# Kernel optimization log

Hardware: AMD Instinct MI355X
Metric: run time of the kernel (lower is better)

The kernel has to match this reference:

```python
import jax, jax.numpy as jnp
import numpy as np
import math

B, N, IN_DIM = 128, 100, 8
E, H, FF, L = 512, 8, 2048, 6
DH = E // H
MAX_STEPS = int(N * 1.5)
EPS = 1e-5

def _ln(x, g, b):
    mu = x.mean(-1, keepdims=True)
    var = ((x - mu) ** 2).mean(-1, keepdims=True)
    return (x - mu) / jnp.sqrt(var + EPS) * g + b

def _mha(q_in, k_in, v_in, wq, bq, wk, bk, wv, bv, wo, bo):
    Bq, Sq = q_in.shape[0], q_in.shape[1]
    q = (q_in @ wq + bq).reshape(Bq, Sq, H, DH)
    k = (k_in @ wk + bk).reshape(Bq, -1, H, DH)
    v = (v_in @ wv + bv).reshape(Bq, -1, H, DH)
    s = jnp.einsum('bqhd,bkhd->bhqk', q, k) / math.sqrt(DH)
    a = jax.nn.softmax(s, axis=-1)
    o = jnp.einsum('bhqk,bkhd->bqhd', a, v).reshape(Bq, Sq, E)
    return o @ wo + bo

def setup_inputs():
    key = jax.random.key(0)
    keys = iter(jax.random.split(key, 64))
    def nrm(shape, s=0.02):
        return jax.random.normal(next(keys), shape, jnp.float32) * s
    d = {}
    d['node_features'] = jax.random.normal(next(keys), (B, N, IN_DIM), jnp.float32)
    d['edge_weights'] = jax.random.uniform(next(keys), (B, N, N), jnp.float32)
    pos = np.arange(N)[:, None].astype(np.float32)
    div = np.exp(np.arange(0, E, 2).astype(np.float32) * (-math.log(10000.0) / E))
    pe = np.zeros((N, E), np.float32)
    pe[:, 0::2] = np.sin(pos * div); pe[:, 1::2] = np.cos(pos * div)
    d['pe'] = jnp.asarray(pe)
    d['in_w'] = nrm((IN_DIM, E)); d['in_b'] = jnp.zeros((E,), jnp.float32)
    for nm in ['enc_wq', 'enc_wk', 'enc_wv', 'enc_wo']:
        d[nm] = nrm((L, E, E))
    for nm in ['enc_bq', 'enc_bk', 'enc_bv', 'enc_bo']:
        d[nm] = jnp.zeros((L, E), jnp.float32)
    d['enc_w1'] = nrm((L, E, FF)); d['enc_b1'] = jnp.zeros((L, FF), jnp.float32)
    d['enc_w2'] = nrm((L, FF, E)); d['enc_b2'] = jnp.zeros((L, E), jnp.float32)
    d['enc_ln1g'] = jnp.ones((L, E), jnp.float32); d['enc_ln1b'] = jnp.zeros((L, E), jnp.float32)
    d['enc_ln2g'] = jnp.ones((L, E), jnp.float32); d['enc_ln2b'] = jnp.zeros((L, E), jnp.float32)
    d['lstm_wih'] = nrm((E, 4 * E)); d['lstm_whh'] = nrm((E, 4 * E))
    d['lstm_bih'] = jnp.zeros((4 * E,), jnp.float32); d['lstm_bhh'] = jnp.zeros((4 * E,), jnp.float32)
    for nm in ['dec_wq', 'dec_wk', 'dec_wv', 'dec_wo', 'dec_pw']:
        d[nm] = nrm((E, E))
    for nm in ['dec_bq', 'dec_bk', 'dec_bv', 'dec_bo', 'dec_pb']:
        d[nm] = jnp.zeros((E,), jnp.float32)
    d['dec_lng'] = jnp.ones((E,), jnp.float32); d['dec_lnb'] = jnp.zeros((E,), jnp.float32)
    d['shortcut_bonus'] = jnp.asarray(5.0, jnp.float32)
    d['revisit_penalty'] = jnp.asarray(-0.5, jnp.float32)
    d['done_w'] = nrm((E, 1)); d['done_b'] = jnp.zeros((1,), jnp.float32)
    return d

def _forward(node_features, edge_weights, pe, in_w, in_b, enc_wq, enc_bq, enc_wk, enc_bk, enc_wv, enc_bv, enc_wo, enc_bo, enc_w1, enc_b1, enc_w2, enc_b2, enc_ln1g, enc_ln1b, enc_ln2g, enc_ln2b, lstm_wih, lstm_whh, lstm_bih, lstm_bhh, dec_wq, dec_bq, dec_wk, dec_bk, dec_wv, dec_bv, dec_wo, dec_bo, dec_pw, dec_pb, dec_lng, dec_lnb, shortcut_bonus, revisit_penalty, done_w, done_b):
    # ---- Encoder (dropout = eval-mode identity) ----
    x = node_features @ in_w + in_b + pe[:N]
    for l in range(L):
        attn = _mha(x, x, x, enc_wq[l], enc_bq[l], enc_wk[l], enc_bk[l], enc_wv[l], enc_bv[l], enc_wo[l], enc_bo[l])
        x = _ln(x + attn, enc_ln1g[l], enc_ln1b[l])
        ff = jax.nn.relu(x @ enc_w1[l] + enc_b1[l]) @ enc_w2[l] + enc_b2[l]
        x = _ln(x + ff, enc_ln2g[l], enc_ln2b[l])
    node_emb = x  # [B, N, E]

    ar = jnp.arange(N)
    ew_to_first = edge_weights[:, :, 0]  # dist(mid -> node 0), [B, N]

    def step_fn(carry, step):
        h, c, ctx, visited, ucount, complete, all_vis, first, prev = carry
        # LSTMCell, torch gate order (i, f, g, o)
        gates = ctx @ lstm_wih + lstm_bih + h @ lstm_whh + lstm_bhh
        i_g, f_g, g_g, o_g = jnp.split(gates, 4, axis=-1)
        c2 = jax.nn.sigmoid(f_g) * c + jax.nn.sigmoid(i_g) * jnp.tanh(g_g)
        h2 = jax.nn.sigmoid(o_g) * jnp.tanh(c2)
        # greedy done-predictor: stop if sigmoid(logit) > 0.5 once tour can be closed
        done_p = jax.nn.sigmoid(h2 @ done_w + done_b)[:, 0]
        eligible = (~complete) & (ucount >= N) & (step >= N)
        complete = complete | (eligible & (done_p > 0.5))
        # DecoderStep: 1-query attention over node embeddings
        a = _mha(h2[:, None, :], node_emb, node_emb, dec_wq, dec_bq, dec_wk, dec_bk, dec_wv, dec_bv, dec_wo, dec_bo)[:, 0]
        a = _ln(a, dec_lng, dec_lnb)
        logits = a @ dec_pw + dec_pb
        scores = jnp.einsum('be,bne->bn', logits, node_emb)
        # revisit penalty while tour incomplete (vectorized masked_fill_)
        scores = jnp.where((~all_vis)[:, None] & visited, revisit_penalty, scores)
        # shortcut bonus once all nodes visited (vectorized gather over edge_weights)
        ew_prev = jnp.take_along_axis(edge_weights, prev[:, None, None], axis=1)[:, 0, :]  # [B, N] row dist(prev -> *)
        direct = ew_prev[:, :1]                      # dist(prev -> 0)
        via = ew_prev + ew_to_first                  # dist(prev -> mid) + dist(mid -> 0)
        bonus = jnp.where(via < direct, shortcut_bonus * (direct - via) / direct, 0.0)
        scores = scores + jnp.where(all_vis[:, None], bonus, 0.0)
        # completed tours: force return to first node
        scores = jnp.where(complete[:, None], -1e9, scores)
        scores = jnp.where(complete[:, None] & (ar[None, :] == first[:, None]), 100.0, scores)
        probs = jax.nn.softmax(scores, axis=1)
        curr = jnp.argmax(probs, axis=1).astype(jnp.int32)  # greedy selection
        logp = jnp.log(jnp.take_along_axis(probs, curr[:, None], 1)[:, 0] + 1e-10)
        first = jnp.where(step == 0, curr, first)
        # state updates (guarded by active, as in the torch per-batch loop)
        active = ~complete
        cur_mask = ar[None, :] == curr[:, None]
        newly = active & ~jnp.take_along_axis(visited, curr[:, None], 1)[:, 0]
        ucount = ucount + newly.astype(jnp.int32)
        visited = visited | (active[:, None] & cur_mask)
        all_vis = all_vis | (ucount >= N)
        ctx2 = jnp.take_along_axis(node_emb, curr[:, None, None], axis=1)[:, 0, :]
        return (h2, c2, ctx2, visited, ucount, complete, all_vis, first, curr), (curr, logp)

    carry0 = (jnp.zeros((B, E), jnp.float32), jnp.zeros((B, E), jnp.float32), node_emb.mean(1),
              jnp.zeros((B, N), bool), jnp.zeros((B,), jnp.int32),
              jnp.zeros((B,), bool), jnp.zeros((B,), bool),
              jnp.zeros((B,), jnp.int32), jnp.zeros((B,), jnp.int32))
    carry, (tours, logps) = jax.lax.scan(step_fn, carry0, jnp.arange(MAX_STEPS))
    complete, first = carry[5], carry[7]
    # final forced step (step == max_steps in torch): incomplete tours return to first node, logp = 0
    final_node = jnp.where(complete, jnp.int32(0), first)
    tours = jnp.concatenate([tours, final_node[None]], 0)                 # [MAX_STEPS+1, B]
    logps = jnp.concatenate([logps, jnp.zeros((1, B), jnp.float32)], 0)   # [MAX_STEPS+1, B]
    return logps, tours

def reference(node_features, edge_weights, pe, in_w, in_b, enc_wq, enc_bq, enc_wk, enc_bk, enc_wv, enc_bv, enc_wo, enc_bo, enc_w1, enc_b1, enc_w2, enc_b2, enc_ln1g, enc_ln1b, enc_ln2g, enc_ln2b, lstm_wih, lstm_whh, lstm_bih, lstm_bhh, dec_wq, dec_bq, dec_wk, dec_bk, dec_wv, dec_bv, dec_wo, dec_bo, dec_pw, dec_pb, dec_lng, dec_lnb, shortcut_bonus, revisit_penalty, done_w, done_b):
    return _forward(node_features, edge_weights, pe, in_w, in_b, enc_wq, enc_bq, enc_wk, enc_bk, enc_wv, enc_bv, enc_wo, enc_bo, enc_w1, enc_b1, enc_w2, enc_b2, enc_ln1g, enc_ln1b, enc_ln2g, enc_ln2b, lstm_wih, lstm_whh, lstm_bih, lstm_bhh, dec_wq, dec_bq, dec_wk, dec_bk, dec_wv, dec_bv, dec_wo, dec_bo, dec_pw, dec_pb, dec_lng, dec_lnb, shortcut_bonus, revisit_penalty, done_w, done_b)
```

## Files before the change

kernel.cpp:

```cpp
#include <hip/hip_runtime.h>
#include <math.h>

#define Bb 128
#define Nn 100
#define Ee 512
#define Hh 8
#define DHd 64
#define FFf 2048
#define Ll 6
#define STEPS 150

typedef _Float16 h8 __attribute__((ext_vector_type(8)));
typedef _Float16 h4 __attribute__((ext_vector_type(4)));
typedef float f4 __attribute__((ext_vector_type(4)));

template<bool RELU, bool BIAS, bool OUTF32, bool SPLITK>
__global__ __launch_bounds__(256) void mgemm_k(
    const _Float16* __restrict__ Ah, const _Float16* __restrict__ Al, int lda,
    const _Float16* __restrict__ Bh, const _Float16* __restrict__ Bl, int ldb,
    float* __restrict__ C, _Float16* __restrict__ Ch, _Float16* __restrict__ Cl,
    int ldc, const float* __restrict__ bias, int K, int kc, int Mtot)
{
  __shared__ _Float16 sm[4 * 5120];
  _Float16* sAh = sm;
// ... 47 lines not shown
      }
    __syncthreads();
  }

  float* Cz = OUTF32 ? (C + (SPLITK ? (size_t)blockIdx.z * (size_t)Mtot * ldc : (size_t)0)) : C;
  int rb = m0 + wm * 64 + kg * 4;
  int cb = n0 + wn * 64 + m16;
#pragma unroll
  for (int j = 0; j < 4; ++j) {
    int col = cb + j * 16;
    float bv = BIAS ? bias[col] : 0.f;
#pragma unroll
    for (int i = 0; i < 4; ++i) {
#pragma unroll
      for (int r = 0; r < 4; ++r) {
        float v = acc[i][j][r] + bv;
        if (RELU) v = fmaxf(v, 0.f);
        int row = rb + i * 16 + r;
        if (OUTF32) {
          Cz[(size_t)row * ldc + col] = v;
        } else {
          _Float16 hh = (_Float16)v;
          Ch[(size_t)row * ldc + col] = hh;
          Cl[(size_t)row * ldc + col] = (_Float16)(v - (float)hh);
        }
      }
    }
  }
}

__global__ __launch_bounds__(256) void wconv_k(
    const float* __restrict__ W, int K, int N,
    _Float16* __restrict__ Th, _Float16* __restrict__ Tl)
{
  __shared__ float t[32][33];
  int n0 = blockIdx.x * 32, k0 = blockIdx.y * 32;
  int tid = threadIdx.x;
  int r = tid >> 3, c4 = (tid & 7) * 4;
  float4 v = *(const float4*)(W + (size_t)(k0 + r) * N + n0 + c4);
  t[r][c4 + 0] = v.x; t[r][c4 + 1] = v.y; t[r][c4 + 2] = v.z; t[r][c4 + 3] = v.w;
  __syncthreads();
  h4 hi, lo;
#pragma unroll
  for (int i = 0; i < 4; ++i) {
    float x = t[c4 + i][r];
    _Float16 hh = (_Float16)x;
    hi[i] = hh;
    lo[i] = (_Float16)(x - (float)hh);
  }
  *(h4*)(Th + (size_t)(n0 + r) * K + k0 + c4) = hi;
  *(h4*)(Tl + (size_t)(n0 + r) * K + k0 + c4) = lo;
}

__global__ __launch_bounds__(256) void reduce4_k(
    const float* __restrict__ P, const float* __restrict__ bias, float* __restrict__ out)
{
  int idx = blockIdx.x * 256 + threadIdx.x;
  const size_t S = 3200ull * 512;
  float v = P[idx] + P[idx + S] + P[idx + 2 * S] + P[idx + 3 * S] + bias[idx & 511];
  out[idx] = v;
}

__global__ __launch_bounds__(256) void input_proj_k(
    const float* __restrict__ nf, const float* __restrict__ inw,
    const float* __restrict__ inb, const float* __restrict__ pe,
    float* __restrict__ x, _Float16* __restrict__ xh, _Float16* __restrict__ xl)
{
  int idx = blockIdx.x * 256 + threadIdx.x;
  int bn = idx >> 9, e = idx & 511;
  int n = bn - (bn / Nn) * Nn;
  const float* fr = nf + (size_t)bn * 8;
  float s = inb[e] + pe[(size_t)n * 512 + e];
#pragma unroll
  for (int i = 0; i < 8; ++i) s += fr[i] * inw[(size_t)i * 512 + e];
  x[idx] = s;
  _Float16 hh = (_Float16)s;
  xh[idx] = hh;
  xl[idx] = (_Float16)(s - (float)hh);
}

__global__ __launch_bounds__(256) void ln_k(
    const float* __restrict__ xin, const float* __restrict__ yin,
    const float* __restrict__ g, const float* __restrict__ bb,
    float* __restrict__ out, _Float16* __restrict__ oh, _Float16* __restrict__ ol)
{
  int row = blockIdx.x, t = threadIdx.x;
  __shared__ float red[256];
  size_t base = (size_t)row * 512;
  float v0 = xin[base + t] + yin[base + t];
  float v1 = xin[base + 256 + t] + yin[base + 256 + t];
  red[t] = v0 + v1;
  __syncthreads();
  for (int o = 128; o > 0; o >>= 1) { if (t < o) red[t] += red[t + o]; __syncthreads(); }
  float mu = red[0] * (1.f / 512.f);
  __syncthreads();
  float d0 = v0 - mu, d1 = v1 - mu;
  red[t] = d0 * d0 + d1 * d1;
  __syncthreads();
  for (int o = 128; o > 0; o >>= 1) { if (t < o) red[t] += red[t + o]; __syncthreads(); }
  float inv = 1.f / sqrtf(red[0] * (1.f / 512.f) + 1e-5f);
  float y0 = d0 * inv * g[t] + bb[t];
  float y1 = d1 * inv * g[t + 256] + bb[t + 256];
  out[base + t] = y0;
  out[base + 256 + t] = y1;
  _Float16 h0 = (_Float16)y0, h1 = (_Float16)y1;
  oh[base + t] = h0;           ol[base + t] = (_Float16)(y0 - (float)h0);
// ... 43 lines not shown
#pragma unroll
    for (int c = 0; c < 7; ++c) {
      int i = i0 + r, j = j0 + c;
      if (i < Nn && j < Nn) p[i * 104 + j] = s[r][c] * 0.125f;
    }
  __syncthreads();
  int w = t >> 6, lane = t & 63;
  for (int i = w; i < Nn; i += 4) {
    float x0 = p[i * 104 + lane];
    float x1 = (lane < 36) ? p[i * 104 + 64 + lane] : -3.4e38f;
    float mx = fmaxf(x0, x1);
    for (int msk = 32; msk; msk >>= 1) mx = fmaxf(mx, __shfl_xor(mx, msk));
    float e0 = expf(x0 - mx);
    float e1 = (lane < 36) ? expf(x1 - mx) : 0.f;
    float ss = e0 + e1;
    for (int msk = 32; msk; msk >>= 1) ss += __shfl_xor(ss, msk);
    p[i * 104 + lane] = e0 / ss;
    if (lane < 36) p[i * 104 + 64 + lane] = e1 / ss;
  }
  __syncthreads();
  int d0 = tj * 4;
  float oa[7][4];
#pragma unroll
  for (int r = 0; r < 7; ++r)
#pragma unroll
    for (int c = 0; c < 4; ++c) oa[r][c] = 0.f;
  for (int j = 0; j < Nn; ++j) {
    float pr[7];
#pragma unroll
    for (int r = 0; r < 7; ++r) pr[r] = p[(i0 + r) * 104 + j];
    float4 vv = *(const float4*)(vg + (size_t)j * 512 + d0);
#pragma unroll
    for (int r = 0; r < 7; ++r) {
      oa[r][0] += pr[r] * vv.x; oa[r][1] += pr[r] * vv.y;
      oa[r][2] += pr[r] * vv.z; oa[r][3] += pr[r] * vv.w;
    }
  }
  size_t ob = ((size_t)b * Nn) * 512 + h * 64 + d0;
#pragma unroll
  for (int r = 0; r < 7; ++r)
    if (i0 + r < Nn) {
      h4 hv, lv;
#pragma unroll
      for (int c = 0; c < 4; ++c) {
        _Float16 hh = (_Float16)oa[r][c];
        hv[c] = hh;
        lv[c] = (_Float16)(oa[r][c] - (float)hh);
      }
      *(h4*)(oh + ob + (size_t)(i0 + r) * 512) = hv;
      *(h4*)(ol + ob + (size_t)(i0 + r) * 512) = lv;
    }
}

template<int BM, int BN, int BK, int TM, int TN>
__global__ __launch_bounds__(256) void gemm_k(
    const float* __restrict__ A, int lda,
    const float* __restrict__ B1, const float* __restrict__ B2, int splitB, int ldb,
    float* __restrict__ C, int ldc, int M, int N, int K, int kChunk)
{
  __shared__ __align__(16) float As[BK][BM + 4];
  __shared__ __align__(16) float Bs[BK][BN + 4];
  const int tid = threadIdx.x;
  const int m0 = blockIdx.y * BM;
  const int n0 = blockIdx.x * BN;
  const int k0 = blockIdx.z * kChunk;
  const int kEnd = k0 + kChunk;
  constexpr int TCOLS = BN / TN;
  const int tm = tid / TCOLS;
  const int tn = tid % TCOLS;
  float acc[TM][TN];
#pragma unroll
  for (int i = 0; i < TM; ++i)
#pragma unroll
    for (int j = 0; j < TN; ++j) acc[i][j] = 0.f;

  for (int kt = k0; kt < kEnd; kt += BK) {
    constexpr int A4 = BM * BK / 4;
    for (int c = tid; c < A4; c += 256) {
      int mm = c / (BK / 4);
      int k4 = (c % (BK / 4)) * 4;
      float4 av = *(const float4*)(A + (size_t)(m0 + mm) * lda + kt + k4);
      As[k4 + 0][mm] = av.x;
      As[k4 + 1][mm] = av.y;
      As[k4 + 2][mm] = av.z;
      As[k4 + 3][mm] = av.w;
    }
    constexpr int B4 = BK * BN / 4;
    for (int c = tid; c < B4; c += 256) {
      int kk = c / (BN / 4);
      int n4 = (c % (BN / 4)) * 4;
      int kgi = kt + kk;
      const float* Brow = (kgi < splitB) ? (B1 + (size_t)kgi * ldb)
                                         : (B2 + (size_t)(kgi - splitB) * ldb);
      *(float4*)&Bs[kk][n4] = *(const float4*)(Brow + n0 + n4);
    }
    __syncthreads();
#pragma unroll
    for (int kk = 0; kk < BK; ++kk) {
      float a[TM], b[TN];
#pragma unroll
      for (int i = 0; i < TM; ++i) a[i] = As[kk][tm * TM + i];
#pragma unroll
      for (int j = 0; j < TN; ++j) b[j] = Bs[kk][tn * TN + j];
#pragma unroll
      for (int i = 0; i < TM; ++i)
#pragma unroll
        for (int j = 0; j < TN; ++j)
          acc[i][j] += a[i] * b[j];
    }
    __syncthreads();
  }

  float* Cout = C + (size_t)blockIdx.z * (size_t)M * ldc;
#pragma unroll
  for (int i = 0; i < TM; ++i) {
    int m = m0 + tm * TM + i;
#pragma unroll
    for (int j = 0; j < TN; j += 4) {
      int n = n0 + tn * TN + j;
      float4 r;
      r.x = acc[i][j + 0]; r.y = acc[i][j + 1]; r.z = acc[i][j + 2]; r.w = acc[i][j + 3];
      *(float4*)(Cout + (size_t)m * ldc + n) = r;
    }
  }
}

__global__ __launch_bounds__(256) void init_k(
    const float* __restrict__ emb, float* __restrict__ ctxh, float* __restrict__ cbuf,
    int* visited, int* ucount, int* complete, int* allvis, int* first, int* prev,
    float* out)
{
  int b = blockIdx.x, t = threadIdx.x;
#pragma unroll
  for (int r = 0; r < 2; ++r) {
    int e = t + 256 * r;
    float s = 0.f;
    for (int i = 0; i < Nn; ++i) s += emb[((size_t)b * Nn + i) * 512 + e];
    ctxh[(size_t)b * 1024 + e] = s / 100.f;
    ctxh[(size_t)b * 1024 + 512 + e] = 0.f;
    cbuf[(size_t)b * 512 + e] = 0.f;
  }
  if (t < Nn) visited[b * Nn + t] = 0;
  if (t == 0) {
    ucount[b] = 0; complete[b] = 0; allvis[b] = 0; first[b] = 0; prev[b] = 0;
    out[150 * Bb + b] = 0.f;
  }
}

__device__ __forceinline__ float sigm(float x) { return 1.f / (1.f + expf(-x)); }

__global__ __launch_bounds__(256) void lstm_pw_k(
    const float* __restrict__ gP, const float* __restrict__ bih, const float* __restrict__ bhh,
    float* __restrict__ ctxh, float* __restrict__ cbuf,
    const float* __restrict__ done_w, const float* __restrict__ done_b,
    int* complete, const int* ucount, int step)
{
  int b = blockIdx.x, t = threadIdx.x;
  __shared__ float red[256];
  const float* g0 = gP + (size_t)b * 2048;
  const float* g1 = gP + 262144 + (size_t)b * 2048;
  float dsum = 0.f;
#pragma unroll
  for (int r = 0; r < 2; ++r) {
    int e = t + 256 * r;
    float ig = g0[e] + g1[e] + bih[e] + bhh[e];
    float fg = g0[e + 512] + g1[e + 512] + bih[e + 512] + bhh[e + 512];
    float gg = g0[e + 1024] + g1[e + 1024] + bih[e + 1024] + bhh[e + 1024];
    float og = g0[e + 1536] + g1[e + 1536] + bih[e + 1536] + bhh[e + 1536];
    float cprev = cbuf[(size_t)b * 512 + e];
    float c2 = sigm(fg) * cprev + sigm(ig) * tanhf(gg);
    float h2 = sigm(og) * tanhf(c2);
    cbuf[(size_t)b * 512 + e] = c2;
    ctxh[(size_t)b * 1024 + 512 + e] = h2;
    dsum += h2 * done_w[e];
  }
  red[t] = dsum; __syncthreads();
  for (int o = 128; o > 0; o >>= 1) { if (t < o) red[t] += red[t + o]; __syncthreads(); }
  if (t == 0) {
    float z = red[0] + done_b[0];
    if (!complete[b] && ucount[b] >= Nn && step >= Nn && z > 0.f) complete[b] = 1;
  }
}

__global__ __launch_bounds__(128) void dec_attn_k(
    const float* __restrict__ qP, const float* __restrict__ bq,
    const float* __restrict__ Kd, const float* __restrict__ Vd,
    float* __restrict__ o)
{
  int bh = blockIdx.x; int b = bh >> 3, h = bh & 7;
  int t = threadIdx.x;
  __shared__ float qh[64];
  __shared__ float p[100];
  __shared__ float red[128];
  if (t < 64) {
    float s = bq[h * 64 + t];
#pragma unroll
    for (int s8 = 0; s8 < 8; ++s8) s += qP[(size_t)s8 * 65536 + (size_t)b * 512 + h * 64 + t];
    qh[t] = s;
  }
  __syncthreads();
  float scv = -3.4e38f;
  if (t < Nn) {
    const float* kr = Kd + ((size_t)b * Nn + t) * 512 + h * 64;
    float s = 0.f;
#pragma unroll
    for (int d = 0; d < 64; ++d) s += qh[d] * kr[d];
    scv = s * 0.125f;
  }
  red[t] = scv; __syncthreads();
  for (int o2 = 64; o2 > 0; o2 >>= 1) { if (t < o2) red[t] = fmaxf(red[t], red[t + o2]); __syncthreads(); }
  float m = red[0]; __syncthreads();
  float ex = (t < Nn) ? expf(scv - m) : 0.f;
  red[t] = ex; __syncthreads();
  for (int o2 = 64; o2 > 0; o2 >>= 1) { if (t < o2) red[t] += red[t + o2]; __syncthreads(); }
  float Z = red[0];
  if (t < Nn) p[t] = ex / Z;
  __syncthreads();
  if (t < 64) {
    float acc = 0.f;
    const float* vr = Vd + (size_t)b * Nn * 512 + h * 64 + t;
    for (int j = 0; j < Nn; ++j) acc += p[j] * vr[(size_t)j * 512];
    o[(size_t)b * 512 + h * 64 + t] = acc;
  }
}

__global__ __launch_bounds__(256) void dec_ln_k(
    const float* __restrict__ woP, const float* __restrict__ bo,
    const float* __restrict__ g, const float* __restrict__ bb,
    float* __restrict__ out)
{
  int b = blockIdx.x, t = threadIdx.x;
  __shared__ float red[256];
  float v[2];
#pragma unroll
  for (int r = 0; r < 2; ++r) {
    int e = t + 256 * r;
    float s = bo[e];
#pragma unroll
    for (int s8 = 0; s8 < 8; ++s8) s += woP[(size_t)s8 * 65536 + (size_t)b * 512 + e];
    v[r] = s;
  }
  red[t] = v[0] + v[1]; __syncthreads();
  for (int o = 128; o > 0; o >>= 1) { if (t < o) red[t] += red[t + o]; __syncthreads(); }
  float mu = red[0] * (1.f / 512.f);
  __syncthreads();
  float d0 = v[0] - mu, d1 = v[1] - mu;
  red[t] = d0 * d0 + d1 * d1; __syncthreads();
  for (int o = 128; o > 0; o >>= 1) { if (t < o) red[t] += red[t + o]; __syncthreads(); }
  float inv = 1.f / sqrtf(red[0] * (1.f / 512.f) + 1e-5f);
  out[(size_t)b * 512 + t] = d0 * inv * g[t] + bb[t];
  out[(size_t)b * 512 + t + 256] = d1 * inv * g[t + 256] + bb[t + 256];
}

__global__ __launch_bounds__(256) void select_k(
    const float* __restrict__ pwP, const float* __restrict__ pb,
    const float* __restrict__ emb, const float* __restrict__ ew,
    int* visited, int* ucount, int* complete, int* allvis, int* first, int* prev,
    float* __restrict__ ctxh, float* __restrict__ out,
    const float* __restrict__ sb_p, const float* __restrict__ rp_p, int step)
{
  int b = blockIdx.x, t = threadIdx.x;
  __shared__ float logits[512];
  __shared__ float sc[128];
  __shared__ float red[256];
  __shared__ int redi[256];
#pragma unroll
  for (int r = 0; r < 2; ++r) {
    int e = t + 256 * r;
    float s = pb[e];
#pragma unroll
    for (int s8 = 0; s8 < 8; ++s8) s += pwP[(size_t)s8 * 65536 + (size_t)b * 512 + e];
    logits[e] = s;
  }
  __syncthreads();
  if (t < Nn) {
    const float* er = emb + ((size_t)b * Nn + t) * 512;
    float s = 0.f;
    for (int e = 0; e < 512; ++e) s += logits[e] * er[e];
    int av = allvis[b];
    if (!av && visited[b * Nn + t]) s = rp_p[0];
    if (av) {
      int pv = prev[b];
      float direct = ew[(size_t)b * 10000 + (size_t)pv * 100];
      float via = ew[(size_t)b * 10000 + (size_t)pv * 100 + t] + ew[(size_t)b * 10000 + (size_t)t * 100];
      if (via < direct) s += sb_p[0] * (direct - via) / direct;
    }
    if (complete[b]) s = (t == first[b]) ? 100.f : -1e9f;
    sc[t] = s;
  }
  __syncthreads();
  float vv = (t < Nn) ? sc[t] : -3.4e38f;
  int ii = (t < Nn) ? t : 0x7fffffff;
  red[t] = vv; redi[t] = ii;
  __syncthreads();
  for (int o = 128; o > 0; o >>= 1) {
    if (t < o) {
      float v2 = red[t + o]; int i2 = redi[t + o];
      if (v2 > red[t] || (v2 == red[t] && i2 < redi[t])) { red[t] = v2; redi[t] = i2; }
    }
    __syncthreads();
  }
  float m = red[0];
  int curr = redi[0];
  __syncthreads();
  float ex = (t < Nn) ? expf(sc[t] - m) : 0.f;
  red[t] = ex; __syncthreads();
  for (int o = 128; o > 0; o >>= 1) { if (t < o) red[t] += red[t + o]; __syncthreads(); }
  float Z = red[0];
  if (t == 0) {
    float pcur = expf(sc[curr] - m) / Z;
    out[step * Bb + b] = logf(pcur + 1e-10f);
    out[(151 + step) * Bb + b] = (float)curr;
    if (!complete[b]) {
      if (!visited[b * Nn + curr]) ucount[b] = ucount[b] + 1;
      visited[b * Nn + curr] = 1;
    }
    if (ucount[b] >= Nn) allvis[b] = 1;
    if (step == 0) first[b] = curr;
    prev[b] = curr;
  }
  const float* src = emb + ((size_t)b * Nn + curr) * 512;
  ctxh[(size_t)b * 1024 + t] = src[t];
  ctxh[(size_t)b * 1024 + t + 256] = src[t + 256];
}

__global__ void final_k(const int* complete, const int* first, float* out)
{
  int b = threadIdx.x;
  out[(151 + 150) * Bb + b] = complete[b] ? 0.f : (float)first[b];
}

extern "C" void kernel_launch(void* const* d_in, const int* in_sizes, int n_in,
                              void* d_out, int out_size, void* d_ws, size_t ws_size,
                              hipStream_t stream)
{
  const float* nf      = (const float*)d_in[0];
  const float* ew      = (const float*)d_in[1];
  const float* pe      = (const float*)d_in[2];
  const float* in_w    = (const float*)d_in[3];
  const float* in_b    = (const float*)d_in[4];
  const float* enc_wq  = (const float*)d_in[5];
  const float* enc_wk  = (const float*)d_in[6];
  const float* enc_wv  = (const float*)d_in[7];
  const float* enc_wo  = (const float*)d_in[8];
  const float* enc_bq  = (const float*)d_in[9];
  const float* enc_bk  = (const float*)d_in[10];
  const float* enc_bv  = (const float*)d_in[11];
  const float* enc_bo  = (const float*)d_in[12];
  const float* enc_w1  = (const float*)d_in[13];
  const float* enc_b1  = (const float*)d_in[14];
  const float* enc_w2  = (const float*)d_in[15];
  const float* enc_b2  = (const float*)d_in[16];
  const float* ln1g    = (const float*)d_in[17];
  const float* ln1b    = (const float*)d_in[18];
  const float* ln2g    = (const float*)d_in[19];
  const float* ln2b    = (const float*)d_in[20];
  const float* wih     = (const float*)d_in[21];
  const float* whh     = (const float*)d_in[22];
  const float* bih     = (const float*)d_in[23];
  const float* bhh     = (const float*)d_in[24];
  const float* dwq     = (const float*)d_in[25];
  const float* dwk     = (const float*)d_in[26];
  const float* dwv     = (const float*)d_in[27];
  const float* dwo     = (const float*)d_in[28];
  const float* dpw     = (const float*)d_in[29];
  const float* dbq     = (const float*)d_in[30];
  const float* dbk     = (const float*)d_in[31];
  const float* dbv     = (const float*)d_in[32];
  const float* dbo     = (const float*)d_in[33];
  const float* dpb     = (const float*)d_in[34];
  const float* dlng    = (const float*)d_in[35];
  const float* dlnb    = (const float*)d_in[36];
  const float* sbp     = (const float*)d_in[37];
  const float* rpp     = (const float*)d_in[38];
  const float* done_w  = (const float*)d_in[39];
  const float* done_b  = (const float*)d_in[40];
  float* out = (float*)d_out;

  const size_t SZ = 12800ull * 512;
  float* ws = (float*)d_ws;
  float* x   = ws;
  float* xq  = x + SZ;
  float* xk  = xq + SZ;
  float* xv  = xk + SZ;
  _Float16* xh = (_Float16*)(xv + SZ);
  _Float16* xl = xh + SZ;
  _Float16* oh = xl + SZ;
  _Float16* ol = oh + SZ;
  _Float16* wb = ol + SZ;
  _Float16* wqh = wb;               _Float16* wql = wqh + 262144;
  _Float16* wkh = wql + 262144;     _Float16* wkl = wkh + 262144;
  _Float16* wvh = wkl + 262144;     _Float16* wvl = wvh + 262144;
  _Float16* woh_ = wvl + 262144;    _Float16* wol_ = woh_ + 262144;
  _Float16* w1h = wol_ + 262144;    _Float16* w1l = w1h + 1048576;
  _Float16* w2h = w1l + 1048576;    _Float16* w2l = w2h + 1048576;
  float* ctxh   = (float*)(w2l + 1048576);
  float* cbuf   = ctxh + 131072;
  float* gatesP = cbuf + 65536;
  float* qP     = gatesP + 524288;
  float* woP    = qP + 524288;
  float* pwP    = woP + 524288;
  float* abuf   = pwP + 524288;
  float* dbuf   = abuf + 65536;
  int* ivis     = (int*)(dbuf + 65536);
  int* ucount   = ivis + 12800;
  int* complete = ucount + 128;
  int* allvis   = complete + 128;
  int* first    = allvis + 128;
  int* prev     = first + 128;

  input_proj_k<<<25600, 256, 0, stream>>>(nf, in_w, in_b, pe, x, xh, xl);

  for (int l = 0; l < Ll; ++l) {
    const float* wq = enc_wq + (size_t)l * 262144;
    const float* wk = enc_wk + (size_t)l * 262144;
    const float* wv = enc_wv + (size_t)l * 262144;
    const float* wo = enc_wo + (size_t)l * 262144;
    const float* bq = enc_bq + (size_t)l * 512;
    const float* bk = enc_bk + (size_t)l * 512;
    const float* bv = enc_bv + (size_t)l * 512;
    const float* bo = enc_bo + (size_t)l * 512;
    const float* w1 = enc_w1 + (size_t)l * 1048576;
    const float* b1 = enc_b1 + (size_t)l * 2048;
    const float* w2 = enc_w2 + (size_t)l * 1048576;
    const float* b2 = enc_b2 + (size_t)l * 512;

    wconv_k<<<dim3(16, 16), 256, 0, stream>>>(wq, 512, 512, wqh, wql);
    wconv_k<<<dim3(16, 16), 256, 0, stream>>>(wk, 512, 512, wkh, wkl);
    wconv_k<<<dim3(16, 16), 256, 0, stream>>>(wv, 512, 512, wvh, wvl);
    wconv_k<<<dim3(16, 16), 256, 0, stream>>>(wo, 512, 512, woh_, wol_);
    wconv_k<<<dim3(64, 16), 256, 0, stream>>>(w1, 512, 2048, w1h, w1l);
    wconv_k<<<dim3(16, 64), 256, 0, stream>>>(w2, 2048, 512, w2h, w2l);

    mgemm_k<false, true, true, false><<<dim3(4, 100), 256, 0, stream>>>(
        xh, xl, 512, wqh, wql, 512, xq, nullptr, nullptr, 512, bq, 512, 0, 0);
    mgemm_k<false, true, true, false><<<dim3(4, 100), 256, 0, stream>>>(
        xh, xl, 512, wkh, wkl, 512, xk, nullptr, nullptr, 512, bk, 512, 0, 0);
    mgemm_k<false, true, true, false><<<dim3(4, 100), 256, 0, stream>>>(
        xh, xl, 512, wvh, wvl, 512, xv, nullptr, nullptr, 512, bv, 512, 0, 0);
    enc_attn_k<<<1024, 256, 0, stream>>>(xq, xk, xv, oh, ol);
    mgemm_k<false, true, true, false><<<dim3(4, 100), 256, 0, stream>>>(
        oh, ol, 512, woh_, wol_, 512, xq, nullptr, nullptr, 512, bo, 512, 0, 0);
    ln_k<<<12800, 256, 0, stream>>>(x, xq, ln1g + l * 512, ln1b + l * 512, x, xh, xl);
    for (int c = 0; c < 4; ++c) {
      mgemm_k<true, true, false, false><<<dim3(16, 25), 256, 0, stream>>>(
          xh + (size_t)c * 3200 * 512, xl + (size_t)c * 3200 * 512, 512,
          w1h, w1l, 512, nullptr, oh, ol, 2048, b1, 512, 0, 0);
      mgemm_k<false, false, true, true><<<dim3(4, 25, 4), 256, 0, stream>>>(
          oh, ol, 2048, w2h, w2l, 2048, xv, nullptr, nullptr, 512,
          nullptr, 2048, 512, 3200);
      reduce4_k<<<6400, 256, 0, stream>>>(xv, b2, xq + (size_t)c * 3200 * 512);
    }
    ln_k<<<12800, 256, 0, stream>>>(x, xq, ln2g + l * 512, ln2b + l * 512, x, xh, xl);
  }

  wconv_k<<<dim3(16, 16), 256, 0, stream>>>(dwk, 512, 512, wqh, wql);
  wconv_k<<<dim3(16, 16), 256, 0, stream>>>(dwv, 512, 512, wkh, wkl);
  mgemm_k<false, true, true, false><<<dim3(4, 100), 256, 0, stream>>>(
      xh, xl, 512, wqh, wql, 512, xk, nullptr, nullptr, 512, dbk, 512, 0, 0);
  mgemm_k<false, true, true, false><<<dim3(4, 100), 256, 0, stream>>>(
      xh, xl, 512, wkh, wkl, 512, xv, nullptr, nullptr, 512, dbv, 512, 0, 0);
  init_k<<<128, 256, 0, stream>>>(x, ctxh, cbuf, ivis, ucount, complete, allvis, first, prev, out);

  for (int step = 0; step < STEPS; ++step) {
    gemm_k<32, 64, 16, 2, 4><<<dim3(32, 4, 2), 256, 0, stream>>>(
        ctxh, 1024, wih, whh, 512, 2048, gatesP, 2048, 128, 2048, 1024, 512);
    lstm_pw_k<<<128, 256, 0, stream>>>(gatesP, bih, bhh, ctxh, cbuf, done_w, done_b,
                                       complete, ucount, step);
    gemm_k<32, 64, 16, 2, 4><<<dim3(8, 4, 8), 256, 0, stream>>>(
        ctxh + 512, 1024, dwq, dwq, 1 << 30, 512, qP, 512, 128, 512, 512, 64);
    dec_attn_k<<<1024, 128, 0, stream>>>(qP, dbq, xk, xv, dbuf);
    gemm_k<32, 64, 16, 2, 4><<<dim3(8, 4, 8), 256, 0, stream>>>(
        dbuf, 512, dwo, dwo, 1 << 30, 512, woP, 512, 128, 512, 512, 64);
    dec_ln_k<<<128, 256, 0, stream>>>(woP, dbo, dlng, dlnb, abuf);
    gemm_k<32, 64, 16, 2, 4><<<dim3(8, 4, 8), 256, 0, stream>>>(
        abuf, 512, dpw, dpw, 1 << 30, 512, pwP, 512, 128, 512, 512, 64);
    select_k<<<128, 256, 0, stream>>>(pwP, dpb, x, ew, ivis, ucount, complete, allvis,
                                      first, prev, ctxh, out, sbp, rpp, step);
  }
  final_k<<<1, 128, 0, stream>>>(complete, first, out);
}
```

Before: 16.52 ms.

## Fuse decoder step kernels: LSTM gates+pointwise, Q-proj+attention, LN folded into pointer projection

After: 30.57 ms. 1.85x slower.

```diff
diff --git a/kernel.cpp b/kernel.cpp
--- a/kernel.cpp
+++ b/kernel.cpp
@@ -123,6 +123,36 @@
   *(h4*)(Tl + (size_t)(n0 + r) * K + k0 + c4) = lo;
 }
 
+__global__ __launch_bounds__(256) void tconv_k(
+    const float* __restrict__ W, int N, const float* __restrict__ gvec,
+    float* __restrict__ T, int ldT, int ko)
+{
+  __shared__ float t[32][33];
+  int n0 = blockIdx.x * 32, k0 = blockIdx.y * 32;
+  int tid = threadIdx.x;
+  int r = tid >> 3, c4 = (tid & 7) * 4;
+  float4 v = *(const float4*)(W + (size_t)(k0 + r) * N + n0 + c4);
+  float s = gvec ? gvec[k0 + r] : 1.f;
+  t[r][c4 + 0] = v.x * s; t[r][c4 + 1] = v.y * s;
+  t[r][c4 + 2] = v.z * s; t[r][c4 + 3] = v.w * s;
+  __syncthreads();
+  float4 o;
+  o.x = t[c4 + 0][r]; o.y = t[c4 + 1][r]; o.z = t[c4 + 2][r]; o.w = t[c4 + 3][r];
+  *(float4*)(T + (size_t)(n0 + r) * ldT + ko + k0 + c4) = o;
+}
+
+__global__ void uv_k(const float* __restrict__ pw, const float* __restrict__ g,
+                     const float* __restrict__ bb, float* __restrict__ uv)
+{
+  int c = blockIdx.x * 256 + threadIdx.x;
+  float su = 0.f, sw = 0.f;
+  for (int k = 0; k < 512; ++k) {
+    float p = pw[(size_t)k * 512 + c];
+    su += g[k] * p; sw += bb[k] * p;
+  }
+  uv[c] = su; uv[512 + c] = sw;
+}
+
 __global__ __launch_bounds__(256) void reduce4_k(
     const float* __restrict__ P, const float* __restrict__ bias, float* __restrict__ out)
 {
@@ -272,77 +302,253 @@
     }
 }
 
-template<int BM, int BN, int BK, int TM, int TN>
-__global__ __launch_bounds__(256) void gemm_k(
-    const float* __restrict__ A, int lda,
-    const float* __restrict__ B1, const float* __restrict__ B2, int splitB, int ldb,
-    float* __restrict__ C, int ldc, int M, int N, int K, int kChunk)
-{
-  __shared__ __align__(16) float As[BK][BM + 4];
-  __shared__ __align__(16) float Bs[BK][BN + 4];
-  const int tid = threadIdx.x;
-  const int m0 = blockIdx.y * BM;
-  const int n0 = blockIdx.x * BN;
-  const int k0 = blockIdx.z * kChunk;
-  const int kEnd = k0 + kChunk;
-  constexpr int TCOLS = BN / TN;
-  const int tm = tid / TCOLS;
-  const int tn = tid % TCOLS;
-  float acc[TM][TN];
-#pragma unroll
-  for (int i = 0; i < TM; ++i)
-#pragma unroll
-    for (int j = 0; j < TN; ++j) acc[i][j] = 0.f;
-
-  for (int kt = k0; kt < kEnd; kt += BK) {
-    constexpr int A4 = BM * BK / 4;
-    for (int c = tid; c < A4; c += 256) {
-      int mm = c / (BK / 4);
-      int k4 = (c % (BK / 4)) * 4;
-      float4 av = *(const float4*)(A + (size_t)(m0 + mm) * lda + kt + k4);
-      As[k4 + 0][mm] = av.x;
-      As[k4 + 1][mm] = av.y;
-      As[k4 + 2][mm] = av.z;
-      As[k4 + 3][mm] = av.w;
-    }
-    constexpr int B4 = BK * BN / 4;
-    for (int c = tid; c < B4; c += 256) {
-      int kk = c / (BN / 4);
-      int n4 = (c % (BN / 4)) * 4;
-      int kgi = kt + kk;
-      const float* Brow = (kgi < splitB) ? (B1 + (size_t)kgi * ldb)
-                                         : (B2 + (size_t)(kgi - splitB) * ldb);
-      *(float4*)&Bs[kk][n4] = *(const float4*)(Brow + n0 + n4);
+__device__ __forceinline__ float sigm(float x) { return 1.f / (1.f + expf(-x)); }
+
+__device__ __forceinline__ void stage_act(const float* __restrict__ src, int row_stride,
+                                          float* __restrict__ sA, int t)
+{
+#pragma unroll
+  for (int i = 0; i < 8; ++i) {
+    int fi = t + i * 256, bb_ = fi >> 4, k4 = fi & 15;
+    float4 v = *(const float4*)(src + (size_t)bb_ * row_stride + k4 * 4);
+    sA[(k4 * 4 + 0) * 129 + bb_] = v.x;
+    sA[(k4 * 4 + 1) * 129 + bb_] = v.y;
+    sA[(k4 * 4 + 2) * 129 + bb_] = v.z;
+    sA[(k4 * 4 + 3) * 129 + bb_] = v.w;
+  }
+}
+
+__global__ __launch_bounds__(256) void lstm_fused_k(
+    const float* __restrict__ WgT, const float* __restrict__ bih,
+    const float* __restrict__ bhh, float* __restrict__ ctxh,
+    float* __restrict__ cbuf, const float* __restrict__ done_w,
+    float* __restrict__ dpart, int hin)
+{
+  __shared__ float sA[64 * 129];
+  __shared__ float sW[8 * 68];
+  __shared__ float sD[256];
+  const int j = blockIdx.x, t = threadIdx.x;
+  const int e0 = j * 2;
+  const int b = t & 127, half = t >> 7;
+  const int e = e0 + half;
+  float ai = 0.f, af = 0.f, ag = 0.f, ao = 0.f;
+  for (int kt = 0; kt < 1024; kt += 64) {
+    const int koff = (kt >= 512 && hin) ? 512 : 0;
+    stage_act(ctxh + koff + kt, 1536, sA, t);
+    if (t < 128) {
+      int r = t >> 4, k4 = t & 15;
+      int col = (r >> 1) * 512 + e0 + (r & 1);
+      *(float4*)(sW + r * 68 + k4 * 4) = *(const float4*)(WgT + (size_t)col * 1024 + kt + k4 * 4);
     }
     __syncthreads();
-#pragma unroll
-    for (int kk = 0; kk < BK; ++kk) {
-      float a[TM], b[TN];
-#pragma unroll
-      for (int i = 0; i < TM; ++i) a[i] = As[kk][tm * TM + i];
-#pragma unroll
-      for (int j = 0; j < TN; ++j) b[j] = Bs[kk][tn * TN + j];
-#pragma unroll
-      for (int i = 0; i < TM; ++i)
-#pragma unroll
-        for (int j = 0; j < TN; ++j)
-          acc[i][j] += a[i] * b[j];
+    const float* wi = sW + half * 68;
+#pragma unroll 8
+    for (int k = 0; k < 64; ++k) {
+      float a = sA[k * 129 + b];
+      ai += a * wi[k];
+      af += a * wi[136 + k];
+      ag += a * wi[272 + k];
+      ao += a * wi[408 + k];
     }
     __syncthreads();
   }
-
-  float* Cout = C + (size_t)blockIdx.z * (size_t)M * ldc;
-#pragma unroll
-  for (int i = 0; i < TM; ++i) {
-    int m = m0 + tm * TM + i;
-#pragma unroll
-    for (int j = 0; j < TN; j += 4) {
-      int n = n0 + tn * TN + j;
-      float4 r;
-      r.x = acc[i][j + 0]; r.y = acc[i][j + 1]; r.z = acc[i][j + 2]; r.w = acc[i][j + 3];
-      *(float4*)(Cout + (size_t)m * ldc + n) = r;
-    }
-  }
+  float ig = ai + bih[e] + bhh[e];
+  float fg = af + bih[512 + e] + bhh[512 + e];
+  float gg = ag + bih[1024 + e] + bhh[1024 + e];
+  float og = ao + bih[1536 + e] + bhh[1536 + e];
+  float cp = cbuf[(size_t)b * 512 + e];
+  float c2 = sigm(fg) * cp + sigm(ig) * tanhf(gg);
+  float h2 = sigm(og) * tanhf(c2);
+  cbuf[(size_t)b * 512 + e] = c2;
+  ctxh[(size_t)b * 1536 + 1024 - hin * 512 + e] = h2;
+  sD[t] = h2 * done_w[e];
+  __syncthreads();
+  if (t < 128) dpart[(size_t)t * 256 + j] = sD[t] + sD[128 + t];
+}
+
+__global__ __launch_bounds__(256) void qattn_k(
+    const float* __restrict__ ctxh, const float* __restrict__ dwqT,
+    const float* __restrict__ dbq, const float* __restrict__ Kd,
+    const float* __restrict__ Vd, float* __restrict__ attno, int hin)
+{
+  __shared__ float sH[16 * 516];
+  __shared__ float sQ[16 * 68];
+  __shared__ float sP[16 * 112];
+  const int bt = blockIdx.x, h = blockIdx.y;
+  const int b0 = bt * 16, t = threadIdx.x;
+  const int b = t >> 4, ln = t & 15, d4 = ln * 4;
+  const int hbase = 1024 - hin * 512;
+#pragma unroll
+  for (int i = 0; i < 8; ++i) {
+    int fi = t + i * 256, bb_ = fi >> 7, k4 = fi & 127;
+    *(float4*)(sH + bb_ * 516 + k4 * 4) =
+        *(const float4*)(ctxh + (size_t)(b0 + bb_) * 1536 + hbase + k4 * 4);
+  }
+  __syncthreads();
+  float qx = 0.f, qy = 0.f, qz = 0.f, qw = 0.f;
+  const float* W0 = dwqT + (size_t)(h * 64 + d4) * 512;
+  for (int k4 = 0; k4 < 128; ++k4) {
+    float4 hv = *(const float4*)(sH + b * 516 + k4 * 4);
+    float4 w0 = *(const float4*)(W0 + k4 * 4);
+    float4 w1 = *(const float4*)(W0 + 512 + k4 * 4);
+    float4 w2 = *(const float4*)(W0 + 1024 + k4 * 4);
+    float4 w3 = *(const float4*)(W0 + 1536 + k4 * 4);
+    qx += hv.x * w0.x + hv.y * w0.y + hv.z * w0.z + hv.w * w0.w;
+    qy += hv.x * w1.x + hv.y * w1.y + hv.z * w1.z + hv.w * w1.w;
+    qz += hv.x * w2.x + hv.y * w2.y + hv.z * w2.z + hv.w * w2.w;
+    qw += hv.x * w3.x + hv.y * w3.y + hv.z * w3.z + hv.w * w3.w;
+  }
+  sQ[b * 68 + d4 + 0] = qx + dbq[h * 64 + d4 + 0];
+  sQ[b * 68 + d4 + 1] = qy + dbq[h * 64 + d4 + 1];
+  sQ[b * 68 + d4 + 2] = qz + dbq[h * 64 + d4 + 2];
+  sQ[b * 68 + d4 + 3] = qw + dbq[h * 64 + d4 + 3];
+  __syncthreads();
+  float sv[7];
+  float smax = -3.4e38f;
+#pragma unroll
+  for (int ni = 0; ni < 7; ++ni) {
+    int n = ln + ni * 16;
+    float s = -3.4e38f;
+    if (n < Nn) {
+      const float* kr = Kd + ((size_t)(b0 + b) * Nn + n) * 512 + h * 64;
+      float acc = 0.f;
+#pragma unroll
+      for (int d = 0; d < 16; ++d) {
+        float4 kv = *(const float4*)(kr + d * 4);
+        float4 qv = *(const float4*)(sQ + b * 68 + d * 4);
+        acc += qv.x * kv.x + qv.y * kv.y + qv.z * kv.z + qv.w * kv.w;
+      }
+      s = acc * 0.125f;
+    }
+    sv[ni] = s;
+    smax = fmaxf(smax, s);
+  }
+#pragma unroll
+  for (int m = 8; m >= 1; m >>= 1) smax = fmaxf(smax, __shfl_xor(smax, m));
+  float ssum = 0.f;
+#pragma unroll
+  for (int ni = 0; ni < 7; ++ni) {
+    int n = ln + ni * 16;
+    if (n < Nn) { sv[ni] = expf(sv[ni] - smax); ssum += sv[ni]; }
+  }
+#pragma unroll
+  for (int m = 8; m >= 1; m >>= 1) ssum += __shfl_xor(ssum, m);
+  float rz = 1.f / ssum;
+#pragma unroll
+  for (int ni = 0; ni < 7; ++ni) {
+    int n = ln + ni * 16;
+    if (n < Nn) sP[b * 112 + n] = sv[ni] * rz;
+  }
+  __syncthreads();
+  float ox = 0.f, oy = 0.f, oz = 0.f, ow = 0.f;
+  const float* vr = Vd + ((size_t)(b0 + b) * Nn) * 512 + h * 64 + d4;
+  for (int n = 0; n < Nn; ++n) {
+    float p = sP[b * 112 + n];
+    float4 vv = *(const float4*)(vr + (size_t)n * 512);
+    ox += p * vv.x; oy += p * vv.y; oz += p * vv.z; ow += p * vv.w;
+  }
+  float4 o4 = {ox, oy, oz, ow};
+  *(float4*)(attno + (size_t)(b0 + b) * 512 + h * 64 + d4) = o4;
+}
+
+__global__ __launch_bounds__(256) void wo_k(
+    const float* __restrict__ A, const float* __restrict__ WT,
+    const float* __restrict__ bias, float* __restrict__ Y,
+    float* __restrict__ lnpart)
+{
+  __shared__ float sA[64 * 129];
+  __shared__ float sW[8 * 68];
+  __shared__ float sS1[256];
+  __shared__ float sS2[256];
+  const int j = blockIdx.x, t = threadIdx.x;
+  const int n0 = j * 8;
+  const int b = t & 127, half = t >> 7;
+  float a0 = 0.f, a1 = 0.f, a2 = 0.f, a3 = 0.f;
+  for (int kt = 0; kt < 512; kt += 64) {
+    stage_act(A + kt, 512, sA, t);
+    if (t < 128) {
+      int r = t >> 4, k4 = t & 15;
+      *(float4*)(sW + r * 68 + k4 * 4) = *(const float4*)(WT + (size_t)(n0 + r) * 512 + kt + k4 * 4);
+    }
+    __syncthreads();
+    const float* wr = sW + half * 272;
+#pragma unroll 8
+    for (int k = 0; k < 64; ++k) {
+      float a = sA[k * 129 + b];
+      a0 += a * wr[k];
+      a1 += a * wr[68 + k];
+      a2 += a * wr[136 + k];
+      a3 += a * wr[204 + k];
+    }
+    __syncthreads();
+  }
+  int c0 = n0 + half * 4;
+  float y0 = a0 + bias[c0 + 0], y1 = a1 + bias[c0 + 1];
+  float y2 = a2 + bias[c0 + 2], y3 = a3 + bias[c0 + 3];
+  float4 y4 = {y0, y1, y2, y3};
+  *(float4*)(Y + (size_t)b * 512 + c0) = y4;
+  sS1[t] = y0 + y1 + y2 + y3;
+  sS2[t] = y0 * y0 + y1 * y1 + y2 * y2 + y3 * y3;
+  __syncthreads();
+  if (t < 128) {
+    float2 pr;
+    pr.x = sS1[t] + sS1[128 + t];
+    pr.y = sS2[t] + sS2[128 + t];
+    *(float2*)(lnpart + ((size_t)j * 128 + t) * 2) = pr;
+  }
+}
+
+__global__ __launch_bounds__(256) void pwln_k(
+    const float* __restrict__ A, const float* __restrict__ WT,
+    const float* __restrict__ lnpart, const float* __restrict__ uv,
+    const float* __restrict__ dpb, float* __restrict__ L)
+{
+  __shared__ float sA[64 * 129];
+  __shared__ float sW[8 * 68];
+  __shared__ float sMu[128];
+  __shared__ float sInv[128];
+  const int j = blockIdx.x, t = threadIdx.x;
+  const int n0 = j * 8;
+  const int b = t & 127, half = t >> 7;
+  if (t < 128) {
+    float s1 = 0.f, s2 = 0.f;
+    const float2* lp = (const float2*)lnpart;
+    for (int jj = 0; jj < 64; ++jj) {
+      float2 pr = lp[jj * 128 + t];
+      s1 += pr.x; s2 += pr.y;
+    }
+    float mu = s1 * (1.f / 512.f);
+    float var = s2 * (1.f / 512.f) - mu * mu;
+    sMu[t] = mu;
+    sInv[t] = 1.f / sqrtf(var + 1e-5f);
+  }
+  float a0 = 0.f, a1 = 0.f, a2 = 0.f, a3 = 0.f;
+  for (int kt = 0; kt < 512; kt += 64) {
+    stage_act(A + kt, 512, sA, t);
+    if (t < 128) {
+      int r = t >> 4, k4 = t & 15;
+      *(float4*)(sW + r * 68 + k4 * 4) = *(const float4*)(WT + (size_t)(n0 + r) * 512 + kt + k4 * 4);
+    }
+    __syncthreads();
+    const float* wr = sW + half * 272;
+#pragma unroll 8
+    for (int k = 0; k < 64; ++k) {
+      float a = sA[k * 129 + b];
+      a0 += a * wr[k];
+      a1 += a * wr[68 + k];
+      a2 += a * wr[136 + k];
+      a3 += a * wr[204 + k];
+    }
+    __syncthreads();
+  }
+  int c0 = n0 + half * 4;
+  float mu = sMu[b], inv = sInv[b];
+  float4 o;
+  o.x = inv * a0 - inv * mu * uv[c0 + 0] + uv[512 + c0 + 0] + dpb[c0 + 0];
+  o.y = inv * a1 - inv * mu * uv[c0 + 1] + uv[512 + c0 + 1] + dpb[c0 + 1];
+  o.z = inv * a2 - inv * mu * uv[c0 + 2] + uv[512 + c0 + 2] + dpb[c0 + 2];
+  o.w = inv * a3 - inv * mu * uv[c0 + 3] + uv[512 + c0 + 3] + dpb[c0 + 3];
+  *(float4*)(L + (size_t)b * 512 + c0) = o;
 }
 
 __global__ __launch_bounds__(256) void init_k(
@@ -356,8 +562,8 @@
     int e = t + 256 * r;
     float s = 0.f;
     for (int i = 0; i < Nn; ++i) s += emb[((size_t)b * Nn + i) * 512 + e];
-    ctxh[(size_t)b * 1024 + e] = s / 100.f;
-    ctxh[(size_t)b * 1024 + 512 + e] = 0.f;
+    ctxh[(size_t)b * 1536 + e] = s / 100.f;
+    ctxh[(size_t)b * 1536 + 512 + e] = 0.f;
     cbuf[(size_t)b * 512 + e] = 0.f;
   }
   if (t < Nn) visited[b * Nn + t] = 0;
@@ -367,136 +573,41 @@
   }
 }
 
-__device__ __forceinline__ float sigm(float x) { return 1.f / (1.f + expf(-x)); }
-
-__global__ __launch_bounds__(256) void lstm_pw_k(
-    const float* __restrict__ gP, const float* __restrict__ bih, const float* __restrict__ bhh,
-    float* __restrict__ ctxh, float* __restrict__ cbuf,
-    const float* __restrict__ done_w, const float* __restrict__ done_b,
-    int* complete, const int* ucount, int step)
-{
-  int b = blockIdx.x, t = threadIdx.x;
-  __shared__ float red[256];
-  const float* g0 = gP + (size_t)b * 2048;
-  const float* g1 = gP + 262144 + (size_t)b * 2048;
-  float dsum = 0.f;
-#pragma unroll
-  for (int r = 0; r < 2; ++r) {
-    int e = t + 256 * r;
-    float ig = g0[e] + g1[e] + bih[e] + bhh[e];
-    float fg = g0[e + 512] + g1[e + 512] + bih[e + 512] + bhh[e + 512];
-    float gg = g0[e + 1024] + g1[e + 1024] + bih[e + 1024] + bhh[e + 1024];
-    float og = g0[e + 1536] + g1[e + 1536] + bih[e + 1536] + bhh[e + 1536];
-    float cprev = cbuf[(size_t)b * 512 + e];
-    float c2 = sigm(fg) * cprev + sigm(ig) * tanhf(gg);
-    float h2 = sigm(og) * tanhf(c2);
-    cbuf[(size_t)b * 512 + e] = c2;
-    ctxh[(size_t)b * 1024 + 512 + e] = h2;
-    dsum += h2 * done_w[e];
-  }
-  red[t] = dsum; __syncthreads();
-  for (int o = 128; o > 0; o >>= 1) { if (t < o) red[t] += red[t + o]; __syncthreads(); }
-  if (t == 0) {
-    float z = red[0] + done_b[0];
-    if (!complete[b] && ucount[b] >= Nn && step >= Nn && z > 0.f) complete[b] = 1;
-  }
-}
-
-__global__ __launch_bounds__(128) void dec_attn_k(
-    const float* __restrict__ qP, const float* __restrict__ bq,
-    const float* __restrict__ Kd, const float* __restrict__ Vd,
-    float* __restrict__ o)
-{
-  int bh = blockIdx.x; int b = bh >> 3, h = bh & 7;
-  int t = threadIdx.x;
-  __shared__ float qh[64];
-  __shared__ float p[100];
-  __shared__ float red[128];
-  if (t < 64) {
-    float s = bq[h * 64 + t];
-#pragma unroll
-    for (int s8 = 0; s8 < 8; ++s8) s += qP[(size_t)s8 * 65536 + (size_t)b * 512 + h * 64 + t];
-    qh[t] = s;
-  }
-  __syncthreads();
-  float scv = -3.4e38f;
-  if (t < Nn) {
-    const float* kr = Kd + ((size_t)b * Nn + t) * 512 + h * 64;
-    float s = 0.f;
-#pragma unroll
-    for (int d = 0; d < 64; ++d) s += qh[d] * kr[d];
-    scv = s * 0.125f;
-  }
-  red[t] = scv; __syncthreads();
-  for (int o2 = 64; o2 > 0; o2 >>= 1) { if (t < o2) red[t] = fmaxf(red[t], red[t + o2]); __syncthreads(); }
-  float m = red[0]; __syncthreads();
-  float ex = (t < Nn) ? expf(scv - m) : 0.f;
-  red[t] = ex; __syncthreads();
-  for (int o2 = 64; o2 > 0; o2 >>= 1) { if (t < o2) red[t] += red[t + o2]; __syncthreads(); }
-  float Z = red[0];
-  if (t < Nn) p[t] = ex / Z;
-  __syncthreads();
-  if (t < 64) {
-    float acc = 0.f;
-    const float* vr = Vd + (size_t)b * Nn * 512 + h * 64 + t;
-    for (int j = 0; j < Nn; ++j) acc += p[j] * vr[(size_t)j * 512];
-    o[(size_t)b * 512 + h * 64 + t] = acc;
-  }
-}
-
-__global__ __launch_bounds__(256) void dec_ln_k(
-    const float* __restrict__ woP, const float* __restrict__ bo,
-    const float* __restrict__ g, const float* __restrict__ bb,
-    float* __restrict__ out)
-{
-  int b = blockIdx.x, t = threadIdx.x;
-  __shared__ float red[256];
-  float v[2];
-#pragma unroll
-  for (int r = 0; r < 2; ++r) {
-    int e = t + 256 * r;
-    float s = bo[e];
-#pragma unroll
-    for (int s8 = 0; s8 < 8; ++s8) s += woP[(size_t)s8 * 65536 + (size_t)b * 512 + e];
-    v[r] = s;
-  }
-  red[t] = v[0] + v[1]; __syncthreads();
-  for (int o = 128; o > 0; o >>= 1) { if (t < o) red[t] += red[t + o]; __syncthreads(); }
-  float mu = red[0] * (1.f / 512.f);
-  __syncthreads();
-  float d0 = v[0] - mu, d1 = v[1] - mu;
-  red[t] = d0 * d0 + d1 * d1; __syncthreads();
-  for (int o = 128; o > 0; o >>= 1) { if (t < o) red[t] += red[t + o]; __syncthreads(); }
-  float inv = 1.f / sqrtf(red[0] * (1.f / 512.f) + 1e-5f);
-  out[(size_t)b * 512 + t] = d0 * inv * g[t] + bb[t];
-  out[(size_t)b * 512 + t + 256] = d1 * inv * g[t + 256] + bb[t + 256];
-}
-
-__global__ __launch_bounds__(256) void select_k(
-    const float* __restrict__ pwP, const float* __restrict__ pb,
-    const float* __restrict__ emb, const float* __restrict__ ew,
+__global__ __launch_bounds__(256) void select2_k(
+    const float* __restrict__ L, const float* __restrict__ emb, const float* __restrict__ ew,
+    const float* __restrict__ dpart, const float* __restrict__ done_b,
     int* visited, int* ucount, int* complete, int* allvis, int* first, int* prev,
     float* __restrict__ ctxh, float* __restrict__ out,
     const float* __restrict__ sb_p, const float* __restrict__ rp_p, int step)
 {
   int b = blockIdx.x, t = threadIdx.x;
-  __shared__ float logits[512];
+  __shared__ float lg[512];
   __shared__ float sc[128];
   __shared__ float red[256];
   __shared__ int redi[256];
-#pragma unroll
-  for (int r = 0; r < 2; ++r) {
-    int e = t + 256 * r;
-    float s = pb[e];
-#pragma unroll
-    for (int s8 = 0; s8 < 8; ++s8) s += pwP[(size_t)s8 * 65536 + (size_t)b * 512 + e];
-    logits[e] = s;
+  __shared__ int s_cm;
+  red[t] = dpart[(size_t)b * 256 + t];
+  lg[t] = L[(size_t)b * 512 + t];
+  lg[t + 256] = L[(size_t)b * 512 + 256 + t];
+  __syncthreads();
+  for (int o = 128; o > 0; o >>= 1) { if (t < o) red[t] += red[t + o]; __syncthreads(); }
+  if (t == 0) {
+    int cm = complete[b];
+    if (!cm && ucount[b] >= Nn && step >= Nn && (red[0] + done_b[0]) > 0.f) {
+      cm = 1; complete[b] = 1;
+    }
+    s_cm = cm;
   }
   __syncthreads();
   if (t < Nn) {
     const float* er = emb + ((size_t)b * Nn + t) * 512;
     float s = 0.f;
-    for (int e = 0; e < 512; ++e) s += logits[e] * er[e];
+#pragma unroll 8
+    for (int e4 = 0; e4 < 128; ++e4) {
+      float4 ev = *(const float4*)(er + e4 * 4);
+      float4 lv = *(const float4*)(lg + e4 * 4);
+      s += lv.x * ev.x + lv.y * ev.y + lv.z * ev.z + lv.w * ev.w;
+    }
     int av = allvis[b];
     if (!av && visited[b * Nn + t]) s = rp_p[0];
     if (av) {
@@ -505,7 +616,7 @@
       float via = ew[(size_t)b * 10000 + (size_t)pv * 100 + t] + ew[(size_t)b * 10000 + (size_t)t * 100];
       if (via < direct) s += sb_p[0] * (direct - via) / direct;
     }
-    if (complete[b]) s = (t == first[b]) ? 100.f : -1e9f;
+    if (s_cm) s = (t == first[b]) ? 100.f : -1e9f;
     sc[t] = s;
   }
   __syncthreads();
@@ -531,7 +642,7 @@
     float pcur = expf(sc[curr] - m) / Z;
     out[step * Bb + b] = logf(pcur + 1e-10f);
     out[(151 + step) * Bb + b] = (float)curr;
-    if (!complete[b]) {
+    if (!s_cm) {
       if (!visited[b * Nn + curr]) ucount[b] = ucount[b] + 1;
       visited[b * Nn + curr] = 1;
     }
@@ -540,8 +651,8 @@
     prev[b] = curr;
   }
   const float* src = emb + ((size_t)b * Nn + curr) * 512;
-  ctxh[(size_t)b * 1024 + t] = src[t];
-  ctxh[(size_t)b * 1024 + t + 256] = src[t + 256];
+  ctxh[(size_t)b * 1536 + t] = src[t];
+  ctxh[(size_t)b * 1536 + t + 256] = src[t + 256];
 }
 
 __global__ void final_k(const int* complete, const int* first, float* out)
@@ -615,14 +726,17 @@
   _Float16* w1h = wol_ + 262144;    _Float16* w1l = w1h + 1048576;
   _Float16* w2h = w1l + 1048576;    _Float16* w2l = w2h + 1048576;
   float* ctxh   = (float*)(w2l + 1048576);
-  float* cbuf   = ctxh + 131072;
-  float* gatesP = cbuf + 65536;
-  float* qP     = gatesP + 524288;
-  float* woP    = qP + 524288;
-  float* pwP    = woP + 524288;
-  float* abuf   = pwP + 524288;
-  float* dbuf   = abuf + 65536;
-  int* ivis     = (int*)(dbuf + 65536);
+  float* cbuf   = ctxh + 196608;
+  float* dwqT   = cbuf + 65536;
+  float* dwoT   = dwqT + 262144;
+  float* pwgT   = dwoT + 262144;
+  float* uvv    = pwgT + 262144;
+  float* lnpart = uvv + 1024;
+  float* dpart  = lnpart + 16384;
+  float* attno  = dpart + 32768;
+  float* woO    = attno + 65536;
+  float* lgts   = woO + 65536;
+  int* ivis     = (int*)(lgts + 65536);
   int* ucount   = ivis + 12800;
   int* complete = ucount + 128;
   int* allvis   = complete + 128;
@@ -680,23 +794,24 @@
       xh, xl, 512, wqh, wql, 512, xk, nullptr, nullptr, 512, dbk, 512, 0, 0);
   mgemm_k<false, true, true, false><<<dim3(4, 100), 256, 0, stream>>>(
       xh, xl, 512, wkh, wkl, 512, xv, nullptr, nullptr, 512, dbv, 512, 0, 0);
+
+  float* WgT = (float*)wb;
+  tconv_k<<<dim3(64, 16), 256, 0, stream>>>(wih, 2048, nullptr, WgT, 1024, 0);
+  tconv_k<<<dim3(64, 16), 256, 0, stream>>>(whh, 2048, nullptr, WgT, 1024, 512);
+  tconv_k<<<dim3(16, 16), 256, 0, stream>>>(dwq, 512, nullptr, dwqT, 512, 0);
+  tconv_k<<<dim3(16, 16), 256, 0, stream>>>(dwo, 512, nullptr, dwoT, 512, 0);
+  tconv_k<<<dim3(16, 16), 256, 0, stream>>>(dpw, 512, dlng, pwgT, 512, 0);
+  uv_k<<<2, 256, 0, stream>>>(dpw, dlng, dlnb, uvv);
   init_k<<<128, 256, 0, stream>>>(x, ctxh, cbuf, ivis, ucount, complete, allvis, first, prev, out);
 
   for (int step = 0; step < STEPS; ++step) {
-    gemm_k<32, 64, 16, 2, 4><<<dim3(32, 4, 2), 256, 0, stream>>>(
-        ctxh, 1024, wih, whh, 512, 2048, gatesP, 2048, 128, 2048, 1024, 512);
-    lstm_pw_k<<<128, 256, 0, stream>>>(gatesP, bih, bhh, ctxh, cbuf, done_w, done_b,
-                                       complete, ucount, step);
-    gemm_k<32, 64, 16, 2, 4><<<dim3(8, 4, 8), 256, 0, stream>>>(
-        ctxh + 512, 1024, dwq, dwq, 1 << 30, 512, qP, 512, 128, 512, 512, 64);
-    dec_attn_k<<<1024, 128, 0, stream>>>(qP, dbq, xk, xv, dbuf);
-    gemm_k<32, 64, 16, 2, 4><<<dim3(8, 4, 8), 256, 0, stream>>>(
-        dbuf, 512, dwo, dwo, 1 << 30, 512, woP, 512, 128, 512, 512, 64);
-    dec_ln_k<<<128, 256, 0, stream>>>(woP, dbo, dlng, dlnb, abuf);
-    gemm_k<32, 64, 16, 2, 4><<<dim3(8, 4, 8), 256, 0, stream>>>(
-        abuf, 512, dpw, dpw, 1 << 30, 512, pwP, 512, 128, 512, 512, 64);
-    select_k<<<128, 256, 0, stream>>>(pwP, dpb, x, ew, ivis, ucount, complete, allvis,
-                                      first, prev, ctxh, out, sbp, rpp, step);
+    int hin = step & 1;
+    lstm_fused_k<<<256, 256, 0, stream>>>(WgT, bih, bhh, ctxh, cbuf, done_w, dpart, hin);
+    qattn_k<<<dim3(8, 8), 256, 0, stream>>>(ctxh, dwqT, dbq, xk, xv, attno, hin);
+    wo_k<<<64, 256, 0, stream>>>(attno, dwoT, dbo, woO, lnpart);
+    pwln_k<<<64, 256, 0, stream>>>(woO, pwgT, lnpart, uvv, dpb, lgts);
+    select2_k<<<128, 256, 0, stream>>>(lgts, x, ew, dpart, done_b, ivis, ucount, complete,
+                                       allvis, first, prev, ctxh, out, sbp, rpp, step);
   }
   final_k<<<1, 128, 0, stream>>>(complete, first, out);
 }
```
